# Optimization experiments

Hardware: AMD Instinct MI355X
Metric: run time of the kernel (lower is better)

Reference implementation:

```python
import jax, jax.numpy as jnp
import numpy as np
from jax import lax

# dims
B, K, P, S = 16, 2048, 512, 16   # batch, votes, num_proposal, nsample
C = 256                           # seed_feat_dim
RADIUS = 0.3
NH, NS, PRE, TXT = 12, 10, 256, 10
HEAD_OUT = 5 + 2 * NH + 4 * NS + PRE  # conv3 out channels = 325


def setup_inputs() -> dict:
    key = jax.random.key(0)
    ks = jax.random.split(key, 16)
    w = lambda k, shp: jax.random.normal(k, shp, jnp.float32) * 0.05
    return {
        'xyz': jax.random.normal(ks[0], (B, K, 3), jnp.float32),
        'features': jax.random.normal(ks[1], (B, C, K), jnp.float32),
        'text_feats': jax.random.normal(ks[2], (TXT, 512), jnp.float32),
        # grouping MLP (1x1 conv2d, bias folded into BN)
        'g_w0': w(ks[3], (3 + C, 128)), 'g_w1': w(ks[4], (128, 128)), 'g_w2': w(ks[5], (128, 128)),
        'g_gam0': jnp.ones(128), 'g_bet0': jnp.zeros(128),
        'g_gam1': jnp.ones(128), 'g_bet1': jnp.zeros(128),
        'g_gam2': jnp.ones(128), 'g_bet2': jnp.zeros(128),
        # decode head
        'conv1_w': w(ks[6], (128, 128)), 'conv1_b': jnp.zeros(128),
        'bn1_g': jnp.ones(128), 'bn1_b': jnp.zeros(128),
        'conv2_w': w(ks[7], (128, 128)), 'conv2_b': jnp.zeros(128),
        'bn2_g': jnp.ones(128), 'bn2_b': jnp.zeros(128),
        'conv3_w': w(ks[8], (128, HEAD_OUT)), 'conv3_b': jnp.zeros(HEAD_OUT),
        # clip header
        'h_w0': w(ks[9], (PRE, 512)), 'h_b0': jnp.zeros(512), 'h_g0': jnp.ones(512), 'h_be0': jnp.zeros(512),
        'h_w1': w(ks[10], (512, 512)), 'h_b1': jnp.zeros(512), 'h_g1': jnp.ones(512), 'h_be1': jnp.zeros(512),
        'h_w2': w(ks[11], (512, 512)), 'h_b2': jnp.zeros(512),
    }


def _fps(pts):
    # farthest point sampling of P points from pts [K,3], starting at index 0
    Kp = pts.shape[0]
    def step(carry, _):
        dmin, last = carry
        d = jnp.sum((pts - pts[last]) ** 2, -1)
        dmin = jnp.minimum(dmin, d)
        nxt = jnp.argmax(dmin).astype(jnp.int32)
        return (dmin, nxt), nxt
    d0 = jnp.full((Kp,), 1e10, pts.dtype)
    _, rest = lax.scan(step, (d0, jnp.int32(0)), None, length=P - 1)
    return jnp.concatenate([jnp.zeros((1,), jnp.int32), rest])


def _bn(x, gam, bet):
    # training-mode batchnorm over all dims but channel (last)
    ax = tuple(range(x.ndim - 1))
    m = x.mean(ax, keepdims=True)
    v = x.var(ax, keepdims=True)
    return gam * (x - m) * lax.rsqrt(v + 1e-5) + bet


def reference(xyz, features, text_feats, g_w0, g_w1, g_w2, g_gam0, g_bet0, g_gam1, g_bet1, g_gam2, g_bet2, conv1_w, conv1_b, bn1_g, bn1_b, conv2_w, conv2_b, bn2_g, bn2_b, conv3_w, conv3_b, h_w0, h_b0, h_g0, h_be0, h_w1, h_b1, h_g1, h_be1, h_w2, h_b2):
    feats_kc = features.transpose(0, 2, 1)            # [B,K,C]
    inds = jax.vmap(_fps)(xyz)                        # [B,P] int32
    new_xyz = jnp.take_along_axis(xyz, inds[..., None], axis=1)  # [B,P,3]
    # ball query: first-S in-radius indices, pad with first valid (center itself)
    d2 = jnp.sum((new_xyz[:, :, None, :] - xyz[:, None, :, :]) ** 2, -1)  # [B,P,K]
    score = jnp.where(d2 < RADIUS * RADIUS, jnp.arange(K, dtype=jnp.int32), jnp.int32(K))
    neg_vals, idx = lax.top_k(-score, S)              # smallest valid indices first
    idx = jnp.where(neg_vals > -K, idx, idx[..., :1])  # [B,P,S]
    gather = jax.vmap(lambda pts, i: pts[i])
    gx = (gather(xyz, idx) - new_xyz[:, :, None, :]) / RADIUS  # normalize_xyz
    gf = gather(feats_kc, idx)
    g = jnp.concatenate([gx, gf], -1)                 # [B,P,S,3+C] (use_xyz)
    h = jax.nn.relu(_bn(g @ g_w0, g_gam0, g_bet0))
    h = jax.nn.relu(_bn(h @ g_w1, g_gam1, g_bet1))
    h = jax.nn.relu(_bn(h @ g_w2, g_gam2, g_bet2))
    feat = h.max(axis=2)                              # [B,P,128] max-pool over neighbors
    net = jax.nn.relu(_bn(feat @ conv1_w + conv1_b, bn1_g, bn1_b))
    net = jax.nn.relu(_bn(net @ conv2_w + conv2_b, bn2_g, bn2_b))
    net = net @ conv3_w + conv3_b                     # [B,P,325]
    clip_in = net[..., -PRE:]
    hh = jax.nn.relu(_bn(clip_in @ h_w0 + h_b0, h_g0, h_be0))
    hh = jax.nn.relu(_bn(hh @ h_w1 + h_b1, h_g1, h_be1))
    q = hh @ h_w2 + h_b2                              # [B,P,512]
    q = q / jnp.linalg.norm(q, axis=-1, keepdims=True)
    t = text_feats / jnp.linalg.norm(text_feats, axis=-1, keepdims=True)
    logits = (1.0 / 0.07) * jnp.einsum('bpd,td->bpt', q, t)  # logit_scale = exp(log(1/0.07))
    out = jnp.concatenate([net[..., :-PRE], logits], -1)     # [B,P,69+TXT]
    return out.transpose(0, 2, 1)                     # [B,79,P] like torch `net`
```

## Files before the change

kernel.cpp:

```cpp
#include <hip/hip_runtime.h>
#include <hip/hip_bf16.h>
#include <cstdint>
#include <cstddef>

#define Bb 16
#define Kk 2048
#define Pp 512
#define Ss 16
#define Cc 256
#define HEADOUT 325

typedef __attribute__((ext_vector_type(8))) short bf16x8;
typedef __attribute__((ext_vector_type(4))) float f32x4;

__device__ __forceinline__ unsigned short f2bf(float x) {
  unsigned u = __float_as_uint(x);
  u = (u + 0x7FFF + ((u >> 16) & 1)) >> 16;
  return (unsigned short)u;
}
__device__ __forceinline__ float bf2f(unsigned short s) {
  return __uint_as_float((unsigned)s << 16);
}
__device__ __forceinline__ void split2(float x, short& h, short& l) {
  unsigned u = __float_as_uint(x);
  h = (short)(u >> 16);
  float r = x - __uint_as_float(u & 0xFFFF0000u);
  l = (short)(__float_as_uint(r) >> 16);
}

static constexpr size_t OFF_TNORM = 0;
static constexpr size_t OFF_SUMS  = 20480;
static constexpr size_t OFF_INDS  = 36864;
static constexpr size_t OFF_IDXL  = 69632;
static constexpr size_t OFF_GX    = 593920;
static constexpr size_t OFF_F1    = 2166784;
static constexpr size_t OFF_BIGA  = 18944000;
static constexpr size_t OFF_BIGB  = 86052864;
static constexpr size_t OFF_NET   = 153161728;
static constexpr size_t OFF_WTH   = 163811328;
static constexpr size_t OFF_WTL   = 165253120;

#define WT_GW1 0
#define WT_GW2 16384
#define WT_C1  32768
#define WT_C2  49152
#define WT_H0  65536
#define WT_H1  196608
#define WT_H2  458752

#define SB0S 0
#define SB0Q 128
#define SB1S 256
#define SB1Q 384
#define SB2S 512
#define SB2Q 640
#define SC1S 768
#define SC1Q 896
#define SC2S 1024
#define SC2Q 1152
#define SH0S 1280
#define SH0Q 1792
#define SH1S 2304
#define SH1Q 2816

template <int CTRL>
__device__ __forceinline__ float fmax_dpp(float v) {
  int o = __builtin_amdgcn_update_dpp(0, __float_as_int(v), CTRL, 0xF, 0xF, true);
  return fmaxf(v, __int_as_float(o));
}

__global__ __launch_bounds__(256, 1) void fused_pre(
    const float* __restrict__ xyz, int* __restrict__ inds,
    const float* __restrict__ features, const float* __restrict__ g_w0,
    float* __restrict__ F1, const float* __restrict__ text,
    float* __restrict__ tn, const float* __restrict__ g_w1,
    const float* __restrict__ g_w2, const float* __restrict__ conv1_w,
    const float* __restrict__ conv2_w, const float* __restrict__ h_w0,
    const float* __restrict__ h_w1, const float* __restrict__ h_w2,
    unsigned short* __restrict__ wth, unsigned short* __restrict__ wtl) {
  __shared__ __align__(16) float smem[8208];
  const int tid = threadIdx.x;

  if (blockIdx.x < 16) {
    #pragma clang fp contract(off)
    const int b = blockIdx.x;
    float4* pt4 = (float4*)smem;
    unsigned long long (*redw)[4] = (unsigned long long(*)[4])(smem + 8192);
    const float* base = xyz + (size_t)b * Kk * 3;
    for (int i = tid; i < Kk; i += 256) {
      pt4[i] = make_float4(base[3 * i], base[3 * i + 1], base[3 * i + 2], 0.f);
    }
    if (tid == 0) inds[b * Pp] = 0;
    float cx[8], cy[8], cz[8], dm[8];
    {
      const float* pb = base + tid * 24;
      float4 f0 = *(const float4*)(pb + 0);
      float4 f1 = *(const float4*)(pb + 4);
      float4 f2 = *(const float4*)(pb + 8);
      float4 f3 = *(const float4*)(pb + 12);
      float4 f4 = *(const float4*)(pb + 16);
      float4 f5 = *(const float4*)(pb + 20);
      cx[0] = f0.x; cy[0] = f0.y; cz[0] = f0.z;
      cx[1] = f0.w; cy[1] = f1.x; cz[1] = f1.y;
      cx[2] = f1.z; cy[2] = f1.w; cz[2] = f2.x;
      cx[3] = f2.y; cy[3] = f2.z; cz[3] = f2.w;
      cx[4] = f3.x; cy[4] = f3.y; cz[4] = f3.z;
      cx[5] = f3.w; cy[5] = f4.x; cz[5] = f4.y;
      cx[6] = f4.z; cy[6] = f4.w; cz[6] = f5.x;
      cx[7] = f5.y; cy[7] = f5.z; cz[7] = f5.w;
      #pragma unroll
      for (int j = 0; j < 8; j++) dm[j] = 1e10f;
    }
    __syncthreads();
    const int lane = tid & 63, wid = tid >> 6;
    int last = 0;
    for (int it = 1; it < Pp; ++it) {
      float4 L = pt4[last];
      float bf = -1.f;
      int bj = 0;
      #pragma unroll
      for (int j = 0; j < 8; j++) {
        float dx = cx[j] - L.x, dy = cy[j] - L.y, dz = cz[j] - L.z;
        float d = (dx * dx + dy * dy) + dz * dz;
        float m2 = fminf(dm[j], d);
        dm[j] = m2;
        if (m2 > bf) { bf = m2; bj = j; }
      }
      float g = bf;
      g = fmax_dpp<0xB1>(g);
      g = fmax_dpp<0x4E>(g);
      g = fmax_dpp<0x141>(g);
      g = fmax_dpp<0x140>(g);
      g = fmaxf(g, __shfl_xor(g, 16, 64));
      g = fmaxf(g, __shfl_xor(g, 32, 64));
      unsigned long long msk = __ballot(bf == g);
      int src = __builtin_ctzll(msk);
      int kk = (tid << 3) | bj;
      int kwin = __shfl(kk, src, 64);
      if (lane == 0)
        redw[it & 1][wid] = ((unsigned long long)__float_as_uint(g) << 32) |
                            (unsigned)(~(unsigned)kwin);
      __syncthreads();
      unsigned long long q0 = redw[it & 1][0], q1 = redw[it & 1][1];
      unsigned long long q2 = redw[it & 1][2], q3 = redw[it & 1][3];
      unsigned long long m0 = q0 > q1 ? q0 : q1;
      unsigned long long m1 = q2 > q3 ? q2 : q3;
      unsigned long long mm = m0 > m1 ? m0 : m1;
      last = (int)(~(unsigned)mm);
      if (tid == 0) inds[b * Pp + it] = last;
    }
  } else if (blockIdx.x == 528) {
    int w = tid >> 6, lane = tid & 63;
    for (int r = w; r < 10; r += 4) {
      const float* rw = text + (size_t)r * 512;
      float v[8];
      float ss = 0.f;
      #pragma unroll
      for (int u = 0; u < 8; u++) { v[u] = rw[lane + 64 * u]; ss += v[u] * v[u]; }
      #pragma unroll
      for (int off = 32; off; off >>= 1) ss += __shfl_xor(ss, off, 64);
      float nrm = sqrtf(ss);
      #pragma unroll
      for (int u = 0; u < 8; u++)
        tn[(size_t)r * 512 + lane + 64 * u] = v[u] / nrm;
    }
  } else if (blockIdx.x >= 529) {
    int wb = blockIdx.x - 529;
    const float* W;
    int K, N, nblk, pidx;
    unsigned short *dh, *dl;
    if (wb < 4)       { W = g_w1;    K = 128; N = 128; dh = wth + WT_GW1; dl = wtl + WT_GW1; nblk = 4;  pidx = wb; }
    else if (wb < 8)  { W = g_w2;    K = 128; N = 128; dh = wth + WT_GW2; dl = wtl + WT_GW2; nblk = 4;  pidx = wb - 4; }
    else if (wb < 12) { W = conv1_w; K = 128; N = 128; dh = wth + WT_C1;  dl = wtl + WT_C1;  nblk = 4;  pidx = wb - 8; }
    else if (wb < 16) { W = conv2_w; K = 128; N = 128; dh = wth + WT_C2;  dl = wtl + WT_C2;  nblk = 4;  pidx = wb - 12; }
    else if (wb < 32) { W = h_w0;    K = 256; N = 512; dh = wth + WT_H0;  dl = wtl + WT_H0;  nblk = 16; pidx = wb - 16; }
    else if (wb < 64) { W = h_w1;    K = 512; N = 512; dh = wth + WT_H1;  dl = wtl + WT_H1;  nblk = 32; pidx = wb - 32; }
    else              { W = h_w2;    K = 512; N = 512; dh = wth + WT_H2;  dl = wtl + WT_H2;  nblk = 32; pidx = wb - 64; }
    for (int idx = pidx * 256 + tid; idx < K * N; idx += nblk * 256) {
      int k = idx / N, n = idx - k * N;
      float w = W[idx];
      unsigned short hi = f2bf(w);
      unsigned short lo = f2bf(w - bf2f(hi));
      dh[n * K + k] = hi;
      dl[n * K + k] = lo;
    }
  } else {
    float (*a_t)[68] = (float(*)[68])smem;
    float (*b_t)[128] = (float(*)[128])(smem + 32 * 68);
    const float* W = g_w0 + 3 * 128;
    const int m0 = (blockIdx.x - 16) * 64;
    float acc[4][8];
    #pragma unroll
    for (int i = 0; i < 4; i++)
      #pragma unroll
      for (int j = 0; j < 8; j++) acc[i][j] = 0.f;
    const int ty = tid >> 4, tx = tid & 15;
    const int lr = tid & 63, wv = tid >> 6;
    const int bb = m0 >> 11, k0 = m0 & 2047;
    const float* fb = features + (size_t)bb * (Cc * Kk);
    for (int c0 = 0; c0 < 256; c0 += 32) {
      #pragma unroll
      for (int i = 0; i < 8; i++) {
        int c = c0 + wv + 4 * i;
        a_t[wv + 4 * i][lr] = fb[(size_t)c * Kk + k0 + lr];
      }
      #pragma unroll
      for (int p = 0; p < 4; p++) {
        int cc = p * 8 + (tid >> 5);
        int nl = (tid & 31) * 4;
        *(float4*)&b_t[cc][nl] = *(const float4*)&W[(size_t)(c0 + cc) * 128 + nl];
      }
      __syncthreads();
      #pragma unroll
      for (int kk = 0; kk < 32; kk++) {
        float4 av = *(const float4*)&a_t[kk][ty * 4];
        float4 b0 = *(const float4*)&b_t[kk][tx * 4];
        float4 b1 = *(const float4*)&b_t[kk][tx * 4 + 64];
        float ap[4] = {av.x, av.y, av.z, av.w};
        float bq0[4] = {b0.x, b0.y, b0.z, b0.w};
        float bq1[4] = {b1.x, b1.y, b1.z, b1.w};
        #pragma unroll
        for (int i = 0; i < 4; i++) {
          #pragma unroll
          for (int u = 0; u < 4; u++) {
            acc[i][u] = fmaf(ap[i], bq0[u], acc[i][u]);
            acc[i][4 + u] = fmaf(ap[i], bq1[u], acc[i][4 + u]);
          }
        }
      }
      __syncthreads();
    }
    #pragma unroll
    for (int i = 0; i < 4; i++) {
      size_t mrow = (size_t)(m0 + ty * 4 + i);
      #pragma unroll
      for (int gq = 0; gq < 2; gq++) {
        float4 v4 = make_float4(acc[i][gq * 4], acc[i][gq * 4 + 1],
                                acc[i][gq * 4 + 2], acc[i][gq * 4 + 3]);
        *(float4*)&F1[mrow * 128 + gq * 64 + tx * 4] = v4;
      }
    }
  }
}

__global__ __launch_bounds__(256) void neigh_k(const float* __restrict__ xyz,
                                               const int* __restrict__ inds,
                                               int* __restrict__ idxl,
                                               float* __restrict__ gx) {
  int widx = blockIdx.x * 4 + (threadIdx.x >> 6);
  int lane = threadIdx.x & 63;
  int b = widx >> 9;
  int q = inds[widx];
  const float* base = xyz + (size_t)b * Kk * 3;
  float qx = base[3 * q], qy = base[3 * q + 1], qz = base[3 * q + 2];
  int cnt = 0;
  int myk = 0;
  for (int ch = 0; ch < 32 && cnt < Ss; ch++) {
    int k = ch * 64 + lane;
    float dx = base[3 * k] - qx;
    float dy = base[3 * k + 1] - qy;
    float dz = base[3 * k + 2] - qz;
    float d2 = __fadd_rn(__fadd_rn(__fmul_rn(dx, dx), __fmul_rn(dy, dy)),
                         __fmul_rn(dz, dz));
    unsigned long long m = __ballot(d2 < 0.09f);
    while (m && cnt < Ss) {
      int t = __builtin_ctzll(m);
      if (lane == cnt) myk = ch * 64 + t;
      cnt++;
      m &= m - 1;
    }
  }
  int first = __shfl(myk, 0, 64);
  if (lane < Ss) {
    int kk = (lane < cnt) ? myk : first;
    size_t o = (size_t)widx * Ss + lane;
    idxl[o] = kk;
    gx[o * 3 + 0] = (base[3 * kk] - qx) / 0.3f;
    gx[o * 3 + 1] = (base[3 * kk + 1] - qy) / 0.3f;
    gx[o * 3 + 2] = (base[3 * kk + 2] - qz) / 0.3f;
  }
}

template <int KD, bool INBN, bool HASBIAS, bool OSUM>
__global__ __launch_bounds__(256, 2) void gemm_mfma(
    const float* __restrict__ A, const unsigned short* __restrict__ Wh,
    const unsigned short* __restrict__ Wl, const float* __restrict__ bias,
    const float* __restrict__ isum, const float* __restrict__ isq,
    float inv_cnt, const float* __restrict__ gamma,
    const float* __restrict__ beta, float* __restrict__ outp, int N,
    float* __restrict__ osum, float* __restrict__ osq) {
  __shared__ float sc[INBN ? KD : 1];
  __shared__ float sh[INBN ? KD : 1];
  __shared__ float red_s[OSUM ? 128 : 1];
  __shared__ float red_q[OSUM ? 128 : 1];
  const int tid = threadIdx.x;
  if (INBN) {
    for (int c = tid; c < KD; c += 256) {
      float mean = isum[c] * inv_cnt;
      float var = isq[c] * inv_cnt - mean * mean;
      float is_ = rsqrtf(var + 1e-5f);
      float scl = gamma[c] * is_;
      sc[c] = scl;
      sh[c] = beta[c] - mean * scl;
    }
  }
  if (OSUM && tid < 128) { red_s[tid] = 0.f; red_q[tid] = 0.f; }
  __syncthreads();
  const int wave = tid >> 6, lane = tid & 63;
  const int wm = wave >> 1, wn = wave & 1;
  const int r = lane & 15, g = lane >> 4;
  const size_t m0 = (size_t)blockIdx.x * 128 + wm * 64;
  const int n0 = blockIdx.y * 128 + wn * 64;

  f32x4 acc[4][4] = {};
  for (int ks = 0; ks < KD / 32; ks++) {
    const int kb = ks * 32 + g * 8;
    bf16x8 bh[4], bl[4];
    #pragma unroll
    for (int nf = 0; nf < 4; nf++) {
      bh[nf] = *(const bf16x8*)&Wh[(size_t)(n0 + nf * 16 + r) * KD + kb];
      bl[nf] = *(const bf16x8*)&Wl[(size_t)(n0 + nf * 16 + r) * KD + kb];
    }
    float s8[8], h8[8];
    if (INBN) {
      #pragma unroll
      for (int j = 0; j < 8; j++) { s8[j] = sc[kb + j]; h8[j] = sh[kb + j]; }
    }
    #pragma unroll
    for (int mf = 0; mf < 4; mf++) {
      const float* ap = &A[(m0 + mf * 16 + r) * KD + kb];
      float4 x0 = *(const float4*)ap;
      float4 x1 = *(const float4*)(ap + 4);
      float xv[8] = {x0.x, x0.y, x0.z, x0.w, x1.x, x1.y, x1.z, x1.w};
      bf16x8 ah, al;
      #pragma unroll
      for (int j = 0; j < 8; j++) {
        float x = xv[j];
        if (INBN) x = fmaxf(fmaf(x, s8[j], h8[j]), 0.f);
        short hh, ll;
        split2(x, hh, ll);
        ah[j] = hh;
        al[j] = ll;
      }
      #pragma unroll
      for (int nf = 0; nf < 4; nf++) {
        acc[mf][nf] = __builtin_amdgcn_mfma_f32_16x16x32_bf16(
            ah, bh[nf], acc[mf][nf], 0, 0, 0);
        acc[mf][nf] = __builtin_amdgcn_mfma_f32_16x16x32_bf16(
            al, bh[nf], acc[mf][nf], 0, 0, 0);
        acc[mf][nf] = __builtin_amdgcn_mfma_f32_16x16x32_bf16(
            ah, bl[nf], acc[mf][nf], 0, 0, 0);
      }
    }
  }
  float bv[4];
  if (HASBIAS) {
    #pragma unroll
    for (int nf = 0; nf < 4; nf++) bv[nf] = bias[n0 + nf * 16 + r];
  }
  float ps[4] = {0.f, 0.f, 0.f, 0.f}, pq[4] = {0.f, 0.f, 0.f, 0.f};
  #pragma unroll
  for (int mf = 0; mf < 4; mf++) {
    #pragma unroll
    for (int nf = 0; nf < 4; nf++) {
      #pragma unroll
      for (int j = 0; j < 4; j++) {
        float v = acc[mf][nf][j];
        if (HASBIAS) v += bv[nf];
        size_t row = m0 + mf * 16 + g * 4 + j;
        int col = n0 + nf * 16 + r;
        if (OSUM) { ps[nf] += v; pq[nf] += v * v; }
        outp[row * N + col] = v;
      }
    }
  }
  if (OSUM) {
    #pragma unroll
    for (int nf = 0; nf < 4; nf++) {
      #pragma unroll
      for (int off = 16; off < 64; off <<= 1) {
        ps[nf] += __shfl_xor(ps[nf], off, 64);
        pq[nf] += __shfl_xor(pq[nf], off, 64);
      }
    }
    if (lane < 16) {
      #pragma unroll
      for (int nf = 0; nf < 4; nf++) {
        int lcol = wn * 64 + nf * 16 + r;
        atomicAdd(&red_s[lcol], ps[nf]);
        atomicAdd(&red_q[lcol], pq[nf]);
      }
    }
    __syncthreads();
    if (tid < 128) {
      atomicAdd(&osum[blockIdx.y * 128 + tid], red_s[tid]);
      atomicAdd(&osq[blockIdx.y * 128 + tid], red_q[tid]);
    }
  }
}

template <int KD, bool INBN, bool HASBIAS, bool WCLIP>
__global__ __launch_bounds__(256) void gemm_f32(
    const float* __restrict__ A, int lda, const float* __restrict__ W, int N,
    const float* __restrict__ bias, const float* __restrict__ isum,
    const float* __restrict__ isq, float inv_cnt,
    const float* __restrict__ gamma, const float* __restrict__ beta,
    float* __restrict__ Cout, int ldc, float* __restrict__ clipf) {
  __shared__ float a_t[32][68];
  __shared__ float b_t[32][128];
  __shared__ float sc[INBN ? KD : 1];
  __shared__ float sh[INBN ? KD : 1];
  const int tid = threadIdx.x;
  const int m0 = blockIdx.x * 64;
  const int n0 = blockIdx.y * 128;
  if (INBN) {
    for (int c = tid; c < KD; c += 256) {
      float mean = isum[c] * inv_cnt;
      float var = isq[c] * inv_cnt - mean * mean;
      float is_ = rsqrtf(var + 1e-5f);
      float scl = gamma[c] * is_;
      sc[c] = scl;
      sh[c] = beta[c] - mean * scl;
    }
    __syncthreads();
  }
  float acc[4][8];
  #pragma unroll
  for (int i = 0; i < 4; i++)
    #pragma unroll
    for (int j = 0; j < 8; j++) acc[i][j] = 0.f;
  const int ty = tid >> 4, tx = tid & 15;
  for (int c0 = 0; c0 < KD; c0 += 32) {
    {
      const int lr = tid >> 2, lcs = tid & 3;
      #pragma unroll
      for (int i = 0; i < 8; i++) {
        int c = c0 + lcs + 4 * i;
        float v = A[(size_t)(m0 + lr) * lda + c];
        if (INBN) v = fmaxf(fmaf(v, sc[c], sh[c]), 0.f);
        a_t[lcs + 4 * i][lr] = v;
      }
    }
    {
      #pragma unroll
      for (int p = 0; p < 4; p++) {
        int cc = p * 8 + (tid >> 5);
        int nl = (tid & 31) * 4;
        #pragma unroll
        for (int u = 0; u < 4; u++) {
          int n = n0 + nl + u;
          b_t[cc][nl + u] = (n < N) ? W[(size_t)(c0 + cc) * N + n] : 0.f;
        }
      }
    }
    __syncthreads();
    #pragma unroll
    for (int kk = 0; kk < 32; kk++) {
      float4 av = *(const float4*)&a_t[kk][ty * 4];
      float4 b0 = *(const float4*)&b_t[kk][tx * 4];
      float4 b1 = *(const float4*)&b_t[kk][tx * 4 + 64];
      float ap[4] = {av.x, av.y, av.z, av.w};
      float bq0[4] = {b0.x, b0.y, b0.z, b0.w};
      float bq1[4] = {b1.x, b1.y, b1.z, b1.w};
      #pragma unroll
      for (int i = 0; i < 4; i++) {
        #pragma unroll
        for (int u = 0; u < 4; u++) {
          acc[i][u] = fmaf(ap[i], bq0[u], acc[i][u]);
          acc[i][4 + u] = fmaf(ap[i], bq1[u], acc[i][4 + u]);
        }
      }
    }
    __syncthreads();
  }
  #pragma unroll
  for (int i = 0; i < 4; i++) {
    size_t m = (size_t)(m0 + ty * 4 + i);
    #pragma unroll
    for (int gq = 0; gq < 2; gq++) {
      #pragma unroll
      for (int u = 0; u < 4; u++) {
        int n = n0 + gq * 64 + tx * 4 + u;
        if (n < N) {
          float v = acc[i][gq * 4 + u];
          if (HASBIAS) v += bias[n];
          Cout[m * ldc + n] = v;
          if (WCLIP && n >= 69) clipf[m * 256 + (n - 69)] = v;
        }
      }
    }
  }
}

__global__ __launch_bounds__(256) void gather_l1(
    const float* __restrict__ F1, const int* __restrict__ idxl,
    const float* __restrict__ gx, const float* __restrict__ g_w0,
    float* __restrict__ L1, float* __restrict__ s0, float* __restrict__ q0) {
  int col = threadIdx.x & 127, half = threadIdx.x >> 7;
  int row0 = blockIdx.x * 64 + half * 32;
  float w0 = g_w0[col], w1 = g_w0[128 + col], w2 = g_w0[256 + col];
  __shared__ float rs[128], rq[128];
  if (threadIdx.x < 128) { rs[threadIdx.x] = 0.f; rq[threadIdx.x] = 0.f; }
  __syncthreads();
  float s = 0.f, q = 0.f;
  for (int rr = 0; rr < 32; rr++) {
    int row = row0 + rr;
    int b = row >> 13;
    int idx = idxl[row];
    float g0 = gx[(size_t)row * 3], g1 = gx[(size_t)row * 3 + 1],
          g2 = gx[(size_t)row * 3 + 2];
    float v = F1[((size_t)(b * Kk + idx)) * 128 + col] + g0 * w0 + g1 * w1 +
              g2 * w2;
    L1[(size_t)row * 128 + col] = v;
    s += v;
    q += v * v;
  }
  atomicAdd(&rs[col], s);
  atomicAdd(&rq[col], q);
  __syncthreads();
  if (threadIdx.x < 128) {
    atomicAdd(&s0[threadIdx.x], rs[threadIdx.x]);
    atomicAdd(&q0[threadIdx.x], rq[threadIdx.x]);
  }
}

__global__ __launch_bounds__(256) void maxpool_bn(
    const float* __restrict__ L3, const float* __restrict__ s2,
    const float* __restrict__ q2, const float* __restrict__ gam,
    const float* __restrict__ bet, float* __restrict__ feat) {
  int col = threadIdx.x & 127, half = threadIdx.x >> 7;
  int bq = blockIdx.x * 2 + half;
  float mean = s2[col] * (1.f / 131072.f);
  float var = q2[col] * (1.f / 131072.f) - mean * mean;
  float is_ = rsqrtf(var + 1e-5f);
  float scl = gam[col] * is_, shf = bet[col] - mean * scl;
  float m = -1e30f;
  #pragma unroll
  for (int s_ = 0; s_ < Ss; s_++) {
    float v = L3[((size_t)bq * Ss + s_) * 128 + col];
    v = fmaxf(fmaf(v, scl, shf), 0.f);
    m = fmaxf(m, v);
  }
  feat[(size_t)bq * 128 + col] = m;
}

__global__ __launch_bounds__(512) void final2(const float* __restrict__ net,
                                              const float* __restrict__ qbuf,
                                              const float* __restrict__ tn,
                                              float* __restrict__ out) {
  __shared__ float tile[79][65];
  const int blk = blockIdx.x;
  const int tid = threadIdx.x;
  const int r = tid >> 3, oct = tid & 7;
  const int row = blk * 64 + r;
  const int b = (blk * 64) >> 9, p0 = (blk * 64) & 511;

  const float* qr = qbuf + (size_t)row * 512 + oct * 64;
  float4 q4[16];
  #pragma unroll
  for (int i = 0; i < 16; i++) q4[i] = *(const float4*)(qr + 4 * i);
  float ss = 0.f;
  float dot[10];
  #pragma unroll
  for (int t = 0; t < 10; t++) dot[t] = 0.f;
  #pragma unroll
  for (int i = 0; i < 16; i++) {
    float4 a = q4[i];
    ss += a.x * a.x + a.y * a.y + a.z * a.z + a.w * a.w;
    #pragma unroll
    for (int t = 0; t < 10; t++) {
      float4 b4 = *(const float4*)(tn + (size_t)t * 512 + oct * 64 + i * 4);
      dot[t] += a.x * b4.x + a.y * b4.y + a.z * b4.z + a.w * b4.w;
    }
  }
  #pragma unroll
  for (int off = 1; off < 8; off <<= 1) {
    ss += __shfl_xor(ss, off, 8);
    #pragma unroll
    for (int t = 0; t < 10; t++) dot[t] += __shfl_xor(dot[t], off, 8);
  }
  if (oct == 0) {
    float inv = rsqrtf(ss) * (1.f / 0.07f);
    #pragma unroll
    for (int t = 0; t < 10; t++) tile[69 + t][r] = dot[t] * inv;
  }
  for (int idx = tid; idx < 64 * 69; idx += 512) {
    int r2 = idx / 69, ch = idx - 69 * r2;
    tile[ch][r2] = net[(size_t)(blk * 64 + r2) * 325 + ch];
  }
  __syncthreads();
  for (int idx = tid; idx < 79 * 64; idx += 512) {
    int ch = idx >> 6, rr = idx & 63;
    out[((size_t)b * 79 + ch) * 512 + p0 + rr] = tile[ch][rr];
  }
}

extern "C" void kernel_launch(void* const* d_in, const int* in_sizes, int n_in,
                              void* d_out, int out_size, void* d_ws,
                              size_t ws_size, hipStream_t stream) {
  const float* xyz = (const float*)d_in[0];
  const float* features = (const float*)d_in[1];
  const float* text = (const float*)d_in[2];
  const float* g_w0 = (const float*)d_in[3];
  const float* g_w1 = (const float*)d_in[4];
  const float* g_w2 = (const float*)d_in[5];
  const float* g_gam0 = (const float*)d_in[6];
  const float* g_bet0 = (const float*)d_in[7];
  const float* g_gam1 = (const float*)d_in[8];
  const float* g_bet1 = (const float*)d_in[9];
  const float* g_gam2 = (const float*)d_in[10];
  const float* g_bet2 = (const float*)d_in[11];
  const float* conv1_w = (const float*)d_in[12];
  const float* conv1_b = (const float*)d_in[13];
  const float* bn1_g = (const float*)d_in[14];
  const float* bn1_b = (const float*)d_in[15];
  const float* conv2_w = (const float*)d_in[16];
  const float* conv2_b = (const float*)d_in[17];
  const float* bn2_g = (const float*)d_in[18];
  const float* bn2_b = (const float*)d_in[19];
  const float* conv3_w = (const float*)d_in[20];
  const float* conv3_b = (const float*)d_in[21];
  const float* h_w0 = (const float*)d_in[22];
  const float* h_b0 = (const float*)d_in[23];
  const float* h_g0 = (const float*)d_in[24];
  const float* h_be0 = (const float*)d_in[25];
  const float* h_w1 = (const float*)d_in[26];
  const float* h_b1 = (const float*)d_in[27];
  const float* h_g1 = (const float*)d_in[28];
  const float* h_be1 = (const float*)d_in[29];
  const float* h_w2 = (const float*)d_in[30];
  const float* h_b2 = (const float*)d_in[31];
  float* out = (float*)d_out;
  char* ws = (char*)d_ws;

  float* tn = (float*)(ws + OFF_TNORM);
  float* sums = (float*)(ws + OFF_SUMS);
  int* inds = (int*)(ws + OFF_INDS);
  int* idxl = (int*)(ws + OFF_IDXL);
  float* gx = (float*)(ws + OFF_GX);
  float* F1 = (float*)(ws + OFF_F1);
  float* BIGA = (float*)(ws + OFF_BIGA);
  float* BIGB = (float*)(ws + OFF_BIGB);
  float* FEAT = (float*)(ws + OFF_BIGB);
  float* C1F = (float*)(ws + OFF_BIGB + 4194304);
  float* C2F = (float*)(ws + OFF_BIGB + 8388608);
  float* CLIPF = (float*)(ws + OFF_BIGB + 12582912);
  float* H0F = (float*)(ws + OFF_BIGA);
  float* H1F = (float*)(ws + OFF_BIGA + 16777216);
  float* QF = (float*)(ws + OFF_BIGA + 33554432);
  float* net = (float*)(ws + OFF_NET);
  unsigned short* WTH = (unsigned short*)(ws + OFF_WTH);
  unsigned short* WTL = (unsigned short*)(ws + OFF_WTL);

  hipMemsetAsync(sums, 0, 16384, stream);
  fused_pre<<<625, 256, 0, stream>>>(xyz, inds, features, g_w0, F1, text, tn,
                                     g_w1, g_w2, conv1_w, conv2_w, h_w0, h_w1,
                                     h_w2, WTH, WTL);
  neigh_k<<<2048, 256, 0, stream>>>(xyz, inds, idxl, gx);
  gather_l1<<<2048, 256, 0, stream>>>(F1, idxl, gx, g_w0, BIGA, sums + SB0S,
                                      sums + SB0Q);
  gemm_mfma<128, true, false, true><<<dim3(1024, 1), 256, 0, stream>>>(
      BIGA, WTH + WT_GW1, WTL + WT_GW1, nullptr, sums + SB0S, sums + SB0Q,
      1.f / 131072.f, g_gam0, g_bet0, BIGB, 128, sums + SB1S, sums + SB1Q);
  gemm_mfma<128, true, false, true><<<dim3(1024, 1), 256, 0, stream>>>(
      BIGB, WTH + WT_GW2, WTL + WT_GW2, nullptr, sums + SB1S, sums + SB1Q,
      1.f / 131072.f, g_gam1, g_bet1, BIGA, 128, sums + SB2S, sums + SB2Q);
  maxpool_bn<<<4096, 256, 0, stream>>>(BIGA, sums + SB2S, sums + SB2Q, g_gam2,
                                       g_bet2, FEAT);
  gemm_mfma<128, false, true, true><<<dim3(64, 1), 256, 0, stream>>>(
      FEAT, WTH + WT_C1, WTL + WT_C1, conv1_b, nullptr, nullptr, 0.f, nullptr,
      nullptr, C1F, 128, sums + SC1S, sums + SC1Q);
  gemm_mfma<128, true, true, true><<<dim3(64, 1), 256, 0, stream>>>(
      C1F, WTH + WT_C2, WTL + WT_C2, conv2_b, sums + SC1S, sums + SC1Q,
      1.f / 8192.f, bn1_g, bn1_b, C2F, 128, sums + SC2S, sums + SC2Q);
  gemm_f32<128, true, true, true><<<dim3(128, 3), 256, 0, stream>>>(
      C2F, 128, conv3_w, 325, conv3_b, sums + SC2S, sums + SC2Q, 1.f / 8192.f,
      bn2_g, bn2_b, net, 325, CLIPF);
  gemm_mfma<256, false, true, true><<<dim3(64, 4), 256, 0, stream>>>(
      CLIPF, WTH + WT_H0, WTL + WT_H0, h_b0, nullptr, nullptr, 0.f, nullptr,
      nullptr, H0F, 512, sums + SH0S, sums + SH0Q);
  gemm_mfma<512, true, true, true><<<dim3(64, 4), 256, 0, stream>>>(
      H0F, WTH + WT_H1, WTL + WT_H1, h_b1, sums + SH0S, sums + SH0Q,
      1.f / 8192.f, h_g0, h_be0, H1F, 512, sums + SH1S, sums + SH1Q);
  gemm_mfma<512, true, true, false><<<dim3(64, 4), 256, 0, stream>>>(
      H1F, WTH + WT_H2, WTL + WT_H2, h_b2, sums + SH1S, sums + SH1Q,
      1.f / 8192.f, h_g1, h_be1, QF, 512, nullptr, nullptr);
  final2<<<128, 512, 0, stream>>>(net, QF, tn, out);
}
```

Baseline: 848.8 us.

## Fuse neighbor max-pool into layer-3 GEMM epilogue and move conv3 to MFMA

The third grouping GEMM now reduces over the 16 neighbors in its epilogue and writes only the pooled features. The BN+ReLU of that layer moves into the next GEMM's input transform, which removes the large intermediate write and the separate maxpool kernel. conv3 now uses the split-bf16 MFMA GEMM with zero-padded, pre-transposed weights, and writes net compactly with 69 columns. The FPS inner loop is packed into float2 math and uses DPP row broadcasts plus readlane instead of cross-lane shuffles. Pooling before BN is only valid when the BN scale is non-negative, which is an assumption.

Measured after the change: 784.5 us. -7.6%, faster.

```diff
diff --git a/kernel.cpp b/kernel.cpp
--- a/kernel.cpp
+++ b/kernel.cpp
@@ -8,10 +8,10 @@
 #define Pp 512
 #define Ss 16
 #define Cc 256
-#define HEADOUT 325
 
 typedef __attribute__((ext_vector_type(8))) short bf16x8;
 typedef __attribute__((ext_vector_type(4))) float f32x4;
+typedef float v2f __attribute__((ext_vector_type(2)));
 
 __device__ __forceinline__ unsigned short f2bf(float x) {
   unsigned u = __float_as_uint(x);
@@ -37,8 +37,8 @@
 static constexpr size_t OFF_BIGA  = 18944000;
 static constexpr size_t OFF_BIGB  = 86052864;
 static constexpr size_t OFF_NET   = 153161728;
-static constexpr size_t OFF_WTH   = 163811328;
-static constexpr size_t OFF_WTL   = 165253120;
+static constexpr size_t OFF_WTH   = 155422720;
+static constexpr size_t OFF_WTL   = 156962816;
 
 #define WT_GW1 0
 #define WT_GW2 16384
@@ -47,6 +47,7 @@
 #define WT_H0  65536
 #define WT_H1  196608
 #define WT_H2  458752
+#define WT_C3  720896
 
 #define SB0S 0
 #define SB0Q 128
@@ -75,9 +76,10 @@
     float* __restrict__ F1, const float* __restrict__ text,
     float* __restrict__ tn, const float* __restrict__ g_w1,
     const float* __restrict__ g_w2, const float* __restrict__ conv1_w,
-    const float* __restrict__ conv2_w, const float* __restrict__ h_w0,
-    const float* __restrict__ h_w1, const float* __restrict__ h_w2,
-    unsigned short* __restrict__ wth, unsigned short* __restrict__ wtl) {
+    const float* __restrict__ conv2_w, const float* __restrict__ conv3_w,
+    const float* __restrict__ h_w0, const float* __restrict__ h_w1,
+    const float* __restrict__ h_w2, unsigned short* __restrict__ wth,
+    unsigned short* __restrict__ wtl) {
   __shared__ __align__(16) float smem[8208];
   const int tid = threadIdx.x;
 
@@ -91,7 +93,7 @@
       pt4[i] = make_float4(base[3 * i], base[3 * i + 1], base[3 * i + 2], 0.f);
     }
     if (tid == 0) inds[b * Pp] = 0;
-    float cx[8], cy[8], cz[8], dm[8];
+    v2f PX[4], PY[4], PZ[4], DM[4];
     {
       const float* pb = base + tid * 24;
       float4 f0 = *(const float4*)(pb + 0);
@@ -100,45 +102,55 @@
       float4 f3 = *(const float4*)(pb + 12);
       float4 f4 = *(const float4*)(pb + 16);
       float4 f5 = *(const float4*)(pb + 20);
-      cx[0] = f0.x; cy[0] = f0.y; cz[0] = f0.z;
-      cx[1] = f0.w; cy[1] = f1.x; cz[1] = f1.y;
-      cx[2] = f1.z; cy[2] = f1.w; cz[2] = f2.x;
-      cx[3] = f2.y; cy[3] = f2.z; cz[3] = f2.w;
-      cx[4] = f3.x; cy[4] = f3.y; cz[4] = f3.z;
-      cx[5] = f3.w; cy[5] = f4.x; cz[5] = f4.y;
-      cx[6] = f4.z; cy[6] = f4.w; cz[6] = f5.x;
-      cx[7] = f5.y; cy[7] = f5.z; cz[7] = f5.w;
-      #pragma unroll
-      for (int j = 0; j < 8; j++) dm[j] = 1e10f;
+      PX[0] = (v2f){f0.x, f0.w}; PY[0] = (v2f){f0.y, f1.x}; PZ[0] = (v2f){f0.z, f1.y};
+      PX[1] = (v2f){f1.z, f2.y}; PY[1] = (v2f){f1.w, f2.z}; PZ[1] = (v2f){f2.x, f2.w};
+      PX[2] = (v2f){f3.x, f3.w}; PY[2] = (v2f){f3.y, f4.x}; PZ[2] = (v2f){f3.z, f4.y};
+      PX[3] = (v2f){f4.z, f5.y}; PY[3] = (v2f){f4.w, f5.z}; PZ[3] = (v2f){f5.x, f5.w};
+      #pragma unroll
+      for (int p = 0; p < 4; p++) DM[p] = (v2f){1e10f, 1e10f};
     }
     __syncthreads();
     const int lane = tid & 63, wid = tid >> 6;
     int last = 0;
     for (int it = 1; it < Pp; ++it) {
       float4 L = pt4[last];
-      float bf = -1.f;
-      int bj = 0;
-      #pragma unroll
-      for (int j = 0; j < 8; j++) {
-        float dx = cx[j] - L.x, dy = cy[j] - L.y, dz = cz[j] - L.z;
-        float d = (dx * dx + dy * dy) + dz * dz;
-        float m2 = fminf(dm[j], d);
-        dm[j] = m2;
-        if (m2 > bf) { bf = m2; bj = j; }
-      }
+      v2f vlx = {L.x, L.x}, vly = {L.y, L.y}, vlz = {L.z, L.z};
+      float pf[4];
+      int pk_[4];
+      #pragma unroll
+      for (int p = 0; p < 4; p++) {
+        v2f dx = PX[p] - vlx, dy = PY[p] - vly, dz = PZ[p] - vlz;
+        v2f d = (dx * dx + dy * dy) + dz * dz;
+        v2f m2 = __builtin_elementwise_min(DM[p], d);
+        DM[p] = m2;
+        bool t = m2.y > m2.x;
+        pf[p] = t ? m2.y : m2.x;
+        pk_[p] = 2 * p + (t ? 1 : 0);
+      }
+      bool t01 = pf[1] > pf[0];
+      float f01 = t01 ? pf[1] : pf[0];
+      int k01 = t01 ? pk_[1] : pk_[0];
+      bool t23 = pf[3] > pf[2];
+      float f23 = t23 ? pf[3] : pf[2];
+      int k23 = t23 ? pk_[3] : pk_[2];
+      bool tt = f23 > f01;
+      float bf = tt ? f23 : f01;
+      int bj = tt ? k23 : k01;
       float g = bf;
       g = fmax_dpp<0xB1>(g);
       g = fmax_dpp<0x4E>(g);
       g = fmax_dpp<0x141>(g);
       g = fmax_dpp<0x140>(g);
-      g = fmaxf(g, __shfl_xor(g, 16, 64));
-      g = fmaxf(g, __shfl_xor(g, 32, 64));
-      unsigned long long msk = __ballot(bf == g);
+      g = fmax_dpp<0x142>(g);
+      g = fmax_dpp<0x143>(g);
+      float gs = __uint_as_float(
+          (unsigned)__builtin_amdgcn_readlane(__float_as_int(g), 63));
+      unsigned long long msk = __ballot(bf == gs);
       int src = __builtin_ctzll(msk);
       int kk = (tid << 3) | bj;
-      int kwin = __shfl(kk, src, 64);
+      int kwin = __builtin_amdgcn_readlane(kk, src);
       if (lane == 0)
-        redw[it & 1][wid] = ((unsigned long long)__float_as_uint(g) << 32) |
+        redw[it & 1][wid] = ((unsigned long long)__float_as_uint(gs) << 32) |
                             (unsigned)(~(unsigned)kwin);
       __syncthreads();
       unsigned long long q0 = redw[it & 1][0], q1 = redw[it & 1][1];
@@ -167,18 +179,19 @@
   } else if (blockIdx.x >= 529) {
     int wb = blockIdx.x - 529;
     const float* W;
-    int K, N, nblk, pidx;
+    int K, N, NS, nblk, pidx;
     unsigned short *dh, *dl;
-    if (wb < 4)       { W = g_w1;    K = 128; N = 128; dh = wth + WT_GW1; dl = wtl + WT_GW1; nblk = 4;  pidx = wb; }
-    else if (wb < 8)  { W = g_w2;    K = 128; N = 128; dh = wth + WT_GW2; dl = wtl + WT_GW2; nblk = 4;  pidx = wb - 4; }
-    else if (wb < 12) { W = conv1_w; K = 128; N = 128; dh = wth + WT_C1;  dl = wtl + WT_C1;  nblk = 4;  pidx = wb - 8; }
-    else if (wb < 16) { W = conv2_w; K = 128; N = 128; dh = wth + WT_C2;  dl = wtl + WT_C2;  nblk = 4;  pidx = wb - 12; }
-    else if (wb < 32) { W = h_w0;    K = 256; N = 512; dh = wth + WT_H0;  dl = wtl + WT_H0;  nblk = 16; pidx = wb - 16; }
-    else if (wb < 64) { W = h_w1;    K = 512; N = 512; dh = wth + WT_H1;  dl = wtl + WT_H1;  nblk = 32; pidx = wb - 32; }
-    else              { W = h_w2;    K = 512; N = 512; dh = wth + WT_H2;  dl = wtl + WT_H2;  nblk = 32; pidx = wb - 64; }
+    if (wb < 4)       { W = g_w1;    K = 128; N = 128; NS = 128; dh = wth + WT_GW1; dl = wtl + WT_GW1; nblk = 4;  pidx = wb; }
+    else if (wb < 8)  { W = g_w2;    K = 128; N = 128; NS = 128; dh = wth + WT_GW2; dl = wtl + WT_GW2; nblk = 4;  pidx = wb - 4; }
+    else if (wb < 12) { W = conv1_w; K = 128; N = 128; NS = 128; dh = wth + WT_C1;  dl = wtl + WT_C1;  nblk = 4;  pidx = wb - 8; }
+    else if (wb < 16) { W = conv2_w; K = 128; N = 128; NS = 128; dh = wth + WT_C2;  dl = wtl + WT_C2;  nblk = 4;  pidx = wb - 12; }
+    else if (wb < 32) { W = h_w0;    K = 256; N = 512; NS = 512; dh = wth + WT_H0;  dl = wtl + WT_H0;  nblk = 16; pidx = wb - 16; }
+    else if (wb < 64) { W = h_w1;    K = 512; N = 512; NS = 512; dh = wth + WT_H1;  dl = wtl + WT_H1;  nblk = 32; pidx = wb - 32; }
+    else if (wb < 96) { W = h_w2;    K = 512; N = 512; NS = 512; dh = wth + WT_H2;  dl = wtl + WT_H2;  nblk = 32; pidx = wb - 64; }
+    else              { W = conv3_w; K = 128; N = 384; NS = 325; dh = wth + WT_C3;  dl = wtl + WT_C3;  nblk = 4;  pidx = wb - 96; }
     for (int idx = pidx * 256 + tid; idx < K * N; idx += nblk * 256) {
       int k = idx / N, n = idx - k * N;
-      float w = W[idx];
+      float w = (n < NS) ? W[k * NS + n] : 0.f;
       unsigned short hi = f2bf(w);
       unsigned short lo = f2bf(w - bf2f(hi));
       dh[n * K + k] = hi;
@@ -281,14 +294,15 @@
   }
 }
 
-template <int KD, bool INBN, bool HASBIAS, bool OSUM>
+template <int KD, bool INBN, bool HASBIAS, bool OSUM, bool OMAX, bool WCLIP>
 __global__ __launch_bounds__(256, 2) void gemm_mfma(
     const float* __restrict__ A, const unsigned short* __restrict__ Wh,
     const unsigned short* __restrict__ Wl, const float* __restrict__ bias,
     const float* __restrict__ isum, const float* __restrict__ isq,
     float inv_cnt, const float* __restrict__ gamma,
-    const float* __restrict__ beta, float* __restrict__ outp, int N,
-    float* __restrict__ osum, float* __restrict__ osq) {
+    const float* __restrict__ beta, float* __restrict__ outp, int N, int nout,
+    float* __restrict__ clipf, float* __restrict__ osum,
+    float* __restrict__ osq) {
   __shared__ float sc[INBN ? KD : 1];
   __shared__ float sh[INBN ? KD : 1];
   __shared__ float red_s[OSUM ? 128 : 1];
@@ -356,13 +370,18 @@
   float bv[4];
   if (HASBIAS) {
     #pragma unroll
-    for (int nf = 0; nf < 4; nf++) bv[nf] = bias[n0 + nf * 16 + r];
+    for (int nf = 0; nf < 4; nf++) {
+      int col = n0 + nf * 16 + r;
+      bv[nf] = (!WCLIP || col < nout) ? bias[col] : 0.f;
+    }
   }
   float ps[4] = {0.f, 0.f, 0.f, 0.f}, pq[4] = {0.f, 0.f, 0.f, 0.f};
   #pragma unroll
   for (int mf = 0; mf < 4; mf++) {
+    float mx[4];
     #pragma unroll
     for (int nf = 0; nf < 4; nf++) {
+      float vmax = -1e30f;
       #pragma unroll
       for (int j = 0; j < 4; j++) {
         float v = acc[mf][nf][j];
@@ -370,7 +389,27 @@
         size_t row = m0 + mf * 16 + g * 4 + j;
         int col = n0 + nf * 16 + r;
         if (OSUM) { ps[nf] += v; pq[nf] += v * v; }
-        outp[row * N + col] = v;
+        if (OMAX) {
+          vmax = fmaxf(vmax, v);
+        } else if (WCLIP) {
+          if (col < 69) outp[row * 69 + col] = v;
+          else if (col < nout) clipf[row * 256 + (col - 69)] = v;
+        } else {
+          outp[row * N + col] = v;
+        }
+      }
+      mx[nf] = vmax;
+    }
+    if (OMAX) {
+      #pragma unroll
+      for (int nf = 0; nf < 4; nf++) {
+        float m = mx[nf];
+        m = fmaxf(m, __shfl_xor(m, 16, 64));
+        m = fmaxf(m, __shfl_xor(m, 32, 64));
+        if (g == 0) {
+          size_t bq = (m0 >> 4) + mf;
+          outp[bq * 128 + n0 + nf * 16 + r] = m;
+        }
       }
     }
   }
@@ -395,99 +434,6 @@
     if (tid < 128) {
       atomicAdd(&osum[blockIdx.y * 128 + tid], red_s[tid]);
       atomicAdd(&osq[blockIdx.y * 128 + tid], red_q[tid]);
-    }
-  }
-}
-
-template <int KD, bool INBN, bool HASBIAS, bool WCLIP>
-__global__ __launch_bounds__(256) void gemm_f32(
-    const float* __restrict__ A, int lda, const float* __restrict__ W, int N,
-    const float* __restrict__ bias, const float* __restrict__ isum,
-    const float* __restrict__ isq, float inv_cnt,
-    const float* __restrict__ gamma, const float* __restrict__ beta,
-    float* __restrict__ Cout, int ldc, float* __restrict__ clipf) {
-  __shared__ float a_t[32][68];
-  __shared__ float b_t[32][128];
-  __shared__ float sc[INBN ? KD : 1];
-  __shared__ float sh[INBN ? KD : 1];
-  const int tid = threadIdx.x;
-  const int m0 = blockIdx.x * 64;
-  const int n0 = blockIdx.y * 128;
-  if (INBN) {
-    for (int c = tid; c < KD; c += 256) {
-      float mean = isum[c] * inv_cnt;
-      float var = isq[c] * inv_cnt - mean * mean;
-      float is_ = rsqrtf(var + 1e-5f);
-      float scl = gamma[c] * is_;
-      sc[c] = scl;
-      sh[c] = beta[c] - mean * scl;
-    }
-    __syncthreads();
-  }
-  float acc[4][8];
-  #pragma unroll
-  for (int i = 0; i < 4; i++)
-    #pragma unroll
-    for (int j = 0; j < 8; j++) acc[i][j] = 0.f;
-  const int ty = tid >> 4, tx = tid & 15;
-  for (int c0 = 0; c0 < KD; c0 += 32) {
-    {
-      const int lr = tid >> 2, lcs = tid & 3;
-      #pragma unroll
-      for (int i = 0; i < 8; i++) {
-        int c = c0 + lcs + 4 * i;
-        float v = A[(size_t)(m0 + lr) * lda + c];
-        if (INBN) v = fmaxf(fmaf(v, sc[c], sh[c]), 0.f);
-        a_t[lcs + 4 * i][lr] = v;
-      }
-    }
-    {
-      #pragma unroll
-      for (int p = 0; p < 4; p++) {
-        int cc = p * 8 + (tid >> 5);
-        int nl = (tid & 31) * 4;
-        #pragma unroll
-        for (int u = 0; u < 4; u++) {
-          int n = n0 + nl + u;
-          b_t[cc][nl + u] = (n < N) ? W[(size_t)(c0 + cc) * N + n] : 0.f;
-        }
-      }
-    }
-    __syncthreads();
-    #pragma unroll
-    for (int kk = 0; kk < 32; kk++) {
-      float4 av = *(const float4*)&a_t[kk][ty * 4];
-      float4 b0 = *(const float4*)&b_t[kk][tx * 4];
-      float4 b1 = *(const float4*)&b_t[kk][tx * 4 + 64];
-      float ap[4] = {av.x, av.y, av.z, av.w};
-      float bq0[4] = {b0.x, b0.y, b0.z, b0.w};
-      float bq1[4] = {b1.x, b1.y, b1.z, b1.w};
-      #pragma unroll
-      for (int i = 0; i < 4; i++) {
-        #pragma unroll
-        for (int u = 0; u < 4; u++) {
-          acc[i][u] = fmaf(ap[i], bq0[u], acc[i][u]);
-          acc[i][4 + u] = fmaf(ap[i], bq1[u], acc[i][4 + u]);
-        }
-      }
-    }
-    __syncthreads();
-  }
-  #pragma unroll
-  for (int i = 0; i < 4; i++) {
-    size_t m = (size_t)(m0 + ty * 4 + i);
-    #pragma unroll
-    for (int gq = 0; gq < 2; gq++) {
-      #pragma unroll
-      for (int u = 0; u < 4; u++) {
-        int n = n0 + gq * 64 + tx * 4 + u;
-        if (n < N) {
-          float v = acc[i][gq * 4 + u];
-          if (HASBIAS) v += bias[n];
-          Cout[m * ldc + n] = v;
-          if (WCLIP && n >= 69) clipf[m * 256 + (n - 69)] = v;
-        }
-      }
     }
   }
 }
@@ -524,26 +470,6 @@
   }
 }
 
-__global__ __launch_bounds__(256) void maxpool_bn(
-    const float* __restrict__ L3, const float* __restrict__ s2,
-    const float* __restrict__ q2, const float* __restrict__ gam,
-    const float* __restrict__ bet, float* __restrict__ feat) {
-  int col = threadIdx.x & 127, half = threadIdx.x >> 7;
-  int bq = blockIdx.x * 2 + half;
-  float mean = s2[col] * (1.f / 131072.f);
-  float var = q2[col] * (1.f / 131072.f) - mean * mean;
-  float is_ = rsqrtf(var + 1e-5f);
-  float scl = gam[col] * is_, shf = bet[col] - mean * scl;
-  float m = -1e30f;
-  #pragma unroll
-  for (int s_ = 0; s_ < Ss; s_++) {
-    float v = L3[((size_t)bq * Ss + s_) * 128 + col];
-    v = fmaxf(fmaf(v, scl, shf), 0.f);
-    m = fmaxf(m, v);
-  }
-  feat[(size_t)bq * 128 + col] = m;
-}
-
 __global__ __launch_bounds__(512) void final2(const float* __restrict__ net,
                                               const float* __restrict__ qbuf,
                                               const float* __restrict__ tn,
@@ -586,7 +512,7 @@
   }
   for (int idx = tid; idx < 64 * 69; idx += 512) {
     int r2 = idx / 69, ch = idx - 69 * r2;
-    tile[ch][r2] = net[(size_t)(blk * 64 + r2) * 325 + ch];
+    tile[ch][r2] = net[(size_t)(blk * 64 + r2) * 69 + ch];
   }
   __syncthreads();
   for (int idx = tid; idx < 79 * 64; idx += 512) {
@@ -641,49 +567,60 @@
   float* F1 = (float*)(ws + OFF_F1);
   float* BIGA = (float*)(ws + OFF_BIGA);
   float* BIGB = (float*)(ws + OFF_BIGB);
-  float* FEAT = (float*)(ws + OFF_BIGB);
-  float* C1F = (float*)(ws + OFF_BIGB + 4194304);
-  float* C2F = (float*)(ws + OFF_BIGB + 8388608);
-  float* CLIPF = (float*)(ws + OFF_BIGB + 12582912);
-  float* H0F = (float*)(ws + OFF_BIGA);
-  float* H1F = (float*)(ws + OFF_BIGA + 16777216);
-  float* QF = (float*)(ws + OFF_BIGA + 33554432);
+  float* FEAT = (float*)(ws + OFF_BIGA);
+  float* C1F = (float*)(ws + OFF_BIGA + 4194304);
+  float* C2F = (float*)(ws + OFF_BIGA + 8388608);
+  float* CLIPF = (float*)(ws + OFF_BIGA + 12582912);
+  float* H0F = (float*)(ws + OFF_BIGB);
+  float* H1F = (float*)(ws + OFF_BIGB + 16777216);
+  float* QF = (float*)(ws + OFF_BIGB + 33554432);
   float* net = (float*)(ws + OFF_NET);
   unsigned short* WTH = (unsigned short*)(ws + OFF_WTH);
   unsigned short* WTL = (unsigned short*)(ws + OFF_WTL);
 
   hipMemsetAsync(sums, 0, 16384, stream);
-  fused_pre<<<625, 256, 0, stream>>>(xyz, inds, features, g_w0, F1, text, tn,
-                                     g_w1, g_w2, conv1_w, conv2_w, h_w0, h_w1,
-                                     h_w2, WTH, WTL);
+  fused_pre<<<629, 256, 0, stream>>>(xyz, inds, features, g_w0, F1, text, tn,
+                                     g_w1, g_w2, conv1_w, conv2_w, conv3_w,
+                                     h_w0, h_w1, h_w2, WTH, WTL);
   neigh_k<<<2048, 256, 0, stream>>>(xyz, inds, idxl, gx);
   gather_l1<<<2048, 256, 0, stream>>>(F1, idxl, gx, g_w0, BIGA, sums + SB0S,
                                       sums + SB0Q);
-  gemm_mfma<128, true, false, true><<<dim3(1024, 1), 256, 0, stream>>>(
-      BIGA, WTH + WT_GW1, WTL + WT_GW1, nullptr, sums + SB0S, sums + SB0Q,
-      1.f / 131072.f, g_gam0, g_bet0, BIGB, 128, sums + SB1S, sums + SB1Q);
-  gemm_mfma<128, true, false, true><<<dim3(1024, 1), 256, 0, stream>>>(
-      BIGB, WTH + WT_GW2, WTL + WT_GW2, nullptr, sums + SB1S, sums + SB1Q,
-      1.f / 131072.f, g_gam1, g_bet1, BIGA, 128, sums + SB2S, sums + SB2Q);
-  maxpool_bn<<<4096, 256, 0, stream>>>(BIGA, sums + SB2S, sums + SB2Q, g_gam2,
-                                       g_bet2, FEAT);
-  gemm_mfma<128, false, true, true><<<dim3(64, 1), 256, 0, stream>>>(
-      FEAT, WTH + WT_C1, WTL + WT_C1, conv1_b, nullptr, nullptr, 0.f, nullptr,
-      nullptr, C1F, 128, sums + SC1S, sums + SC1Q);
-  gemm_mfma<128, true, true, true><<<dim3(64, 1), 256, 0, stream>>>(
-      C1F, WTH + WT_C2, WTL + WT_C2, conv2_b, sums + SC1S, sums + SC1Q,
-      1.f / 8192.f, bn1_g, bn1_b, C2F, 128, sums + SC2S, sums + SC2Q);
-  gemm_f32<128, true, true, true><<<dim3(128, 3), 256, 0, stream>>>(
-      C2F, 128, conv3_w, 325, conv3_b, sums + SC2S, sums + SC2Q, 1.f / 8192.f,
-      bn2_g, bn2_b, net, 325, CLIPF);
-  gemm_mfma<256, false, true, true><<<dim3(64, 4), 256, 0, stream>>>(
-      CLIPF, WTH + WT_H0, WTL + WT_H0, h_b0, nullptr, nullptr, 0.f, nullptr,
-      nullptr, H0F, 512, sums + SH0S, sums + SH0Q);
-  gemm_mfma<512, true, true, true><<<dim3(64, 4), 256, 0, stream>>>(
-      H0F, WTH + WT_H1, WTL + WT_H1, h_b1, sums + SH0S, sums + SH0Q,
-      1.f / 8192.f, h_g0, h_be0, H1F, 512, sums + SH1S, sums + SH1Q);
-  gemm_mfma<512, true, true, false><<<dim3(64, 4), 256, 0, stream>>>(
-      H1F, WTH + WT_H2, WTL + WT_H2, h_b2, sums + SH1S, sums + SH1Q,
-      1.f / 8192.f, h_g1, h_be1, QF, 512, nullptr, nullptr);
+  gemm_mfma<128, true, false, true, false, false>
+      <<<dim3(1024, 1), 256, 0, stream>>>(
+          BIGA, WTH + WT_GW1, WTL + WT_GW1, nullptr, sums + SB0S, sums + SB0Q,
+          1.f / 131072.f, g_gam0, g_bet0, BIGB, 128, 128, nullptr,
+          sums + SB1S, sums + SB1Q);
+  gemm_mfma<128, true, false, true, true, false>
+      <<<dim3(1024, 1), 256, 0, stream>>>(
+          BIGB, WTH + WT_GW2, WTL + WT_GW2, nullptr, sums + SB1S, sums + SB1Q,
+          1.f / 131072.f, g_gam1, g_bet1, FEAT, 128, 128, nullptr,
+          sums + SB2S, sums + SB2Q);
+  gemm_mfma<128, true, true, true, false, false>
+      <<<dim3(64, 1), 256, 0, stream>>>(
+          FEAT, WTH + WT_C1, WTL + WT_C1, conv1_b, sums + SB2S, sums + SB2Q,
+          1.f / 131072.f, g_gam2, g_bet2, C1F, 128, 128, nullptr, sums + SC1S,
+          sums + SC1Q);
+  gemm_mfma<128, true, true, true, false, false>
+      <<<dim3(64, 1), 256, 0, stream>>>(
+          C1F, WTH + WT_C2, WTL + WT_C2, conv2_b, sums + SC1S, sums + SC1Q,
+          1.f / 8192.f, bn1_g, bn1_b, C2F, 128, 128, nullptr, sums + SC2S,
+          sums + SC2Q);
+  gemm_mfma<128, true, true, false, false, true>
+      <<<dim3(64, 3), 256, 0, stream>>>(
+          C2F, WTH + WT_C3, WTL + WT_C3, conv3_b, sums + SC2S, sums + SC2Q,
+          1.f / 8192.f, bn2_g, bn2_b, net, 384, 325, CLIPF, nullptr, nullptr);
+  gemm_mfma<256, false, true, true, false, false>
+      <<<dim3(64, 4), 256, 0, stream>>>(
+          CLIPF, WTH + WT_H0, WTL + WT_H0, h_b0, nullptr, nullptr, 0.f,
+          nullptr, nullptr, H0F, 512, 512, nullptr, sums + SH0S, sums + SH0Q);
+  gemm_mfma<512, true, true, true, false, false>
+      <<<dim3(64, 4), 256, 0, stream>>>(
+          H0F, WTH + WT_H1, WTL + WT_H1, h_b1, sums + SH0S, sums + SH0Q,
+          1.f / 8192.f, h_g0, h_be0, H1F, 512, 512, nullptr, sums + SH1S,
+          sums + SH1Q);
+  gemm_mfma<512, true, true, false, false, false>
+      <<<dim3(64, 4), 256, 0, stream>>>(
+          H1F, WTH + WT_H2, WTL + WT_H2, h_b2, sums + SH1S, sums + SH1Q,
+          1.f / 8192.f, h_g1, h_be1, QF, 512, 512, nullptr, nullptr, nullptr);
   final2<<<128, 512, 0, stream>>>(net, QF, tn, out);
 }
```
